# Performance work log

Measured on AMD Instinct MI355X. Metric: run time of the kernel, lower is better.

## Reference

```python
import jax, jax.numpy as jnp
import numpy as np

B, S, D = 16, 2048, 256
HEAD_SIZE = 256  # input_size // num_heads = 256 // 1
SCALE = HEAD_SIZE ** -0.5


def setup_inputs() -> dict:
    key = jax.random.key(0)
    ks = jax.random.split(key, 4)
    s = 1.0 / np.sqrt(D)  # typical linear init scale
    return {
        "x": jax.random.normal(ks[0], (B, S, D), dtype=jnp.float32),
        "Wq": jax.random.normal(ks[1], (D, D), dtype=jnp.float32) * s,
        "bq": jnp.zeros((D,), dtype=jnp.float32),
        "Wk": jax.random.normal(ks[2], (D, D), dtype=jnp.float32) * s,
        "bk": jnp.zeros((D,), dtype=jnp.float32),
        "Wv": jax.random.normal(ks[3], (D, D), dtype=jnp.float32) * s,
        "bv": jnp.zeros((D,), dtype=jnp.float32),
    }


def reference(x, Wq, bq, Wk, bk, Wv, bv):
    # Linear projections (torch Linear: x @ W.T + b)
    q = jnp.einsum("bsd,ed->bse", x, Wq) + bq
    k = jnp.einsum("bsd,ed->bse", x, Wk) + bk
    v = jnp.einsum("bsd,ed->bse", x, Wv) + bv
    # Full attention matrix [B, S, S], scaled by head_size^-0.5
    scores = jnp.einsum("bqd,bkd->bqk", q, k) * SCALE
    attn = jax.nn.softmax(scores, axis=-1)
    # dropout is identity in inference/reference mode
    out = jnp.einsum("bqk,bkd->bqd", attn, v)
    return out
```

## Files before the change

### kernel.cpp

```cpp
#include <hip/hip_runtime.h>
#include <hip/hip_bf16.h>
#include <stdint.h>

#define DEV __device__ __forceinline__

typedef __attribute__((ext_vector_type(8))) short bf16x8;
typedef __attribute__((ext_vector_type(4))) short bf16x4;
typedef __attribute__((ext_vector_type(4))) float f32x4;
typedef __attribute__((ext_vector_type(16))) float f32x16;
typedef unsigned short u16;

DEV void gload_lds16(const void* g, void* l) {
    typedef const __attribute__((address_space(1))) unsigned int* gp_t;
    typedef __attribute__((address_space(3))) unsigned int* lp_t;
    __builtin_amdgcn_global_load_lds((gp_t)(uintptr_t)g, (lp_t)(uint32_t)(uintptr_t)l, 16, 0, 0);
}

DEV u16 f2bf(float x) {
    union { __hip_bfloat16 h; u16 u; } c;
    c.h = __float2bfloat16(x);
    return c.u;
}
DEV unsigned pack2bf(float a, float b) {
    union { __hip_bfloat162 h2; unsigned u; } cv;
    cv.h2 = __float22bfloat162_rn(make_float2(a, b));
    return cv.u;
}
DEV float bflo(unsigned u) { union { unsigned u; float f; } c; c.u = u << 16; return c.f; }
DEV float bfhi(unsigned u) { union { unsigned u; float f; } c; c.u = u & 0xffff0000u; return c.f; }

DEV size_t kidx(int kv, int k) {
    return ((size_t)(kv >> 5) * 8192) + ((k >> 4) * 512)
         + (((((k >> 3) & 1) << 5) | (kv & 31)) << 3) + (k & 7);
}
DEV size_t vidx(int d, int kv) {
    return ((size_t)(kv >> 5) * 8192) + (((kv >> 3) & 3) * 2048) + ((d >> 5) * 256)
         + (((((kv >> 2) & 1) << 5) | (d & 31)) << 2) + (kv & 3);
}

__global__ void cast_kernel(const float* __restrict__ src, u16* __restrict__ dst, int n8) {
    int stride = gridDim.x * blockDim.x;
    for (int i = blockIdx.x * blockDim.x + threadIdx.x; i < n8; i += stride) {
        const float4* s = (const float4*)src + (size_t)i * 2;
        float4 a = s[0], b = s[1];
        union { u16 u[8]; uint4 v; } o;
        o.u[0] = f2bf(a.x); o.u[1] = f2bf(a.y); o.u[2] = f2bf(a.z); o.u[3] = f2bf(a.w);
        o.u[4] = f2bf(b.x); o.u[5] = f2bf(b.y); o.u[6] = f2bf(b.z); o.u[7] = f2bf(b.w);
        *((uint4*)dst + i) = o.v;
    }
}

template <int MODE>
DEV void gemm_body(const u16* A, const u16* Bw, const float* bias,
                   u16* out, int m0, int n0)
{
    __shared__ char smA[16384];
    __shared__ char smB[16384];
    const int lane = threadIdx.x & 63;
    const int w    = threadIdx.x >> 6;
    const int wr   = w >> 1, wc = w & 1;
    const int l15  = lane & 15, lg = lane >> 4;

    f32x4 acc[4][4] = {};
    const char* ag = (const char*)A;
    const char* bg = (const char*)Bw;

    for (int kt = 0; kt < 4; ++kt) {
        __syncthreads();
        #pragma unroll
        for (int c = 0; c < 8; ++c) {
            int ch    = w * 8 + c;
            int loc   = ch & 15;
            int p     = loc * 1024 + lane * 16;
            int row   = p >> 7;
            int inner = (p & 127) ^ ((row & 7) << 4);
            const char* src = (ch < 16 ? ag : bg) + row * 512 + kt * 128 + inner;
            char* dst = (ch < 16 ? smA : smB) + loc * 1024;
            gload_lds16(src, dst);
        }
        __syncthreads();
        #pragma unroll
        for (int ks = 0; ks < 2; ++ks) {
            bf16x8 af[4], bfr[4];
            #pragma unroll
            for (int mi = 0; mi < 4; ++mi) {
                int row = wr * 64 + mi * 16 + l15;
                af[mi] = *(const bf16x8*)(smA + ((row * 128 + ks * 64 + lg * 16) ^ ((row & 7) << 4)));
            }
            #pragma unroll
            for (int ni = 0; ni < 4; ++ni) {
                int row = wc * 64 + ni * 16 + l15;
                bfr[ni] = *(const bf16x8*)(smB + ((row * 128 + ks * 64 + lg * 16) ^ ((row & 7) << 4)));
            }
            #pragma unroll
            for (int mi = 0; mi < 4; ++mi)
                #pragma unroll
                for (int ni = 0; ni < 4; ++ni)
                    acc[mi][ni] = __builtin_amdgcn_mfma_f32_16x16x32_bf16(af[mi], bfr[ni], acc[mi][ni], 0, 0, 0);
        }
    }
    #pragma unroll
    for (int mi = 0; mi < 4; ++mi) {
        #pragma unroll
        for (int ni = 0; ni < 4; ++ni) {
            int gc = n0 + wc * 64 + ni * 16 + l15;
            float bc = (MODE == 2) ? 0.f : bias[gc];
            #pragma unroll
            for (int r = 0; r < 4; ++r) {
                int gr = m0 + wr * 64 + mi * 16 + lg * 4 + r;
                float bb = (MODE == 2) ? bias[gr] : bc;
                u16 val = f2bf(acc[mi][ni][r] + bb);
                if (MODE == 0)      out[(size_t)gr * 256 + gc] = val;
                else if (MODE == 1) out[kidx(gr, gc)] = val;
                else                out[vidx(gr, gc)] = val;
            }
        }
    }
}

__global__ __launch_bounds__(256) void proj_qk_kernel(
    const u16* xb, const u16* wqb, const u16* wkb,
    const float* bq, const float* bk, u16* Q, u16* Kf)
{
    int n0 = blockIdx.x * 128;
    int m0 = blockIdx.y * 128;
    int nl = n0 & 255;
    if (n0 < 256)
        gemm_body<0>(xb + (size_t)m0 * 256, wqb + (size_t)nl * 256, bq, Q,  m0, nl);
    else
        gemm_body<1>(xb + (size_t)m0 * 256, wkb + (size_t)nl * 256, bk, Kf, m0, nl);
}

__global__ __launch_bounds__(256) void proj_v_kernel(
    const u16* wvb, const u16* xb, const float* bv, u16* Vf)
{
    int n0 = blockIdx.x * 128;
    int m0 = blockIdx.y * 128;
    gemm_body<2>(wvb + (size_t)m0 * 256, xb + (size_t)n0 * 256, bv, Vf, m0, n0);
}

__global__ __launch_bounds__(256, 2) void attn_kernel(
    const u16* __restrict__ Q, const u16* __restrict__ Kf,
    const u16* __restrict__ Vf, float* __restrict__ out,
    u16* __restrict__ p1, float2* __restrict__ ml)
{
    __shared__ char sm[65536];

    const int lane = threadIdx.x & 63;
    const int w    = threadIdx.x >> 6;
    const int l31  = lane & 31;
    const int g    = lane >> 5;

    const int lin  = blockIdx.x;
    const int b    = (lin & 7) * 2 + ((lin >> 3) & 1);
    const int half = (lin >> 4) & 1;
    const int qt   = lin >> 5;
    const size_t tokbase = (size_t)b * 2048;
    const int q0w  = qt * 128 + w * 32;
    const int kvh  = half * 1024;

    bf16x8 qf[16];
    {
        const char* qrow = (const char*)(Q + (tokbase + q0w + l31) * 256);
        #pragma unroll
        for (int ks = 0; ks < 16; ++ks)
            qf[ks] = *(const bf16x8*)(qrow + ks * 32 + g * 16);
    }

    const char* Kgb = (const char*)Kf + (tokbase + kvh) * 512;
    const char* Vgb = (const char*)Vf + (tokbase + kvh) * 512;
    const uint32_t so = (uint32_t)(w * 4096 + lane * 16);

    auto stage = [&](int t, int sel) {
        const char* kg = Kgb + (size_t)t * 16384 + so;
        const char* vg = Vgb + (size_t)t * 16384 + so;
        char* kl = sm + sel * 32768 + w * 4096;
        char* vl = kl + 16384;
        #pragma unroll
        for (int j = 0; j < 4; ++j) gload_lds16(kg + j * 1024, kl + j * 1024);
        #pragma unroll
        for (int j = 0; j < 4; ++j) gload_lds16(vg + j * 1024, vl + j * 1024);
    };

    f32x16 acc[8] = {};
    float m_run  = -1e30f;
    float l_lane = 0.f;
    const float C = 0.09016844005556021f;

    stage(0, 0);
    __syncthreads();

    for (int t = 0; t < 32; ++t) {
        const int sel = t & 1;
        if (t < 31) stage(t + 1, sel ^ 1);

        const char* kp = sm + sel * 32768 + lane * 16;
        const char* vp = sm + sel * 32768 + 16384 + lane * 8;

        f32x16 sa = {}, sb = {};
        #pragma unroll
        for (int ks = 0; ks < 8; ++ks) {
            bf16x8 kf = *(const bf16x8*)(kp + ks * 1024);
            sa = __builtin_amdgcn_mfma_f32_32x32x16_bf16(kf, qf[ks], sa, 0, 0, 0);
        }
        #pragma unroll
        for (int ks = 8; ks < 16; ++ks) {
            bf16x8 kf = *(const bf16x8*)(kp + ks * 1024);
            sb = __builtin_amdgcn_mfma_f32_32x32x16_bf16(kf, qf[ks], sb, 0, 0, 0);
        }
        f32x16 st = sa + sb;

        float m0 = fmaxf(fmaxf(st[0], st[1]),   fmaxf(st[2], st[3]));
        float m1 = fmaxf(fmaxf(st[4], st[5]),   fmaxf(st[6], st[7]));
        float m2 = fmaxf(fmaxf(st[8], st[9]),   fmaxf(st[10], st[11]));
        float m3 = fmaxf(fmaxf(st[12], st[13]), fmaxf(st[14], st[15]));
        float lmax = fmaxf(fmaxf(m0, m1), fmaxf(m2, m3));

        if (__any(lmax > m_run + 16.f)) {
            float rmax = fmaxf(lmax, __shfl_xor(lmax, 32, 64));
            float m_new = fmaxf(m_run, rmax);
            float rs = exp2f((m_run - m_new) * C);
            #pragma unroll
            for (int dt = 0; dt < 8; ++dt) acc[dt] *= rs;
            l_lane *= rs;
            m_run = m_new;
        }

        const float mc = m_run * C;
        float sum = 0.f;
        #pragma unroll
        for (int i = 0; i < 16; ++i) {
            float e = exp2f(st[i] * C - mc);
            st[i] = e;
            sum += e;
        }
        l_lane += sum;

        union { unsigned u2[2]; bf16x4 v; } pb[4];
        #pragma unroll
        for (int u = 0; u < 4; ++u) {
            pb[u].u2[0] = pack2bf(st[u * 4 + 0], st[u * 4 + 1]);
            pb[u].u2[1] = pack2bf(st[u * 4 + 2], st[u * 4 + 3]);
        }

        #pragma unroll
        for (int u = 0; u < 4; ++u) {
            #pragma unroll
            for (int dt = 0; dt < 8; ++dt) {
                bf16x4 vf = *(const bf16x4*)(vp + u * 4096 + dt * 512);
                asm("v_mfma_f32_32x32x8_bf16 %0, %1, %2, %0"
                    : "+v"(acc[dt]) : "v"(vf), "v"(pb[u].v));
            }
        }

        __syncthreads();
    }

    float l_row = l_lane + __shfl_xor(l_lane, 32, 64);
    if (g == 0)
        ml[half * 32768 + (int)tokbase + q0w + l31] = make_float2(m_run, l_row);

    float* ow = (float*)(sm + w * 8448);
    #pragma unroll
    for (int p = 0; p < 4; ++p) {
        #pragma unroll
        for (int dt2 = 0; dt2 < 2; ++dt2) {
            const int dt = p * 2 + dt2;
            #pragma unroll
            for (int r = 0; r < 16; ++r) {
                int dl = dt2 * 32 + (r & 3) + 8 * (r >> 2) + 4 * g;
                ow[l31 * 66 + dl] = acc[dt][r];
            }
        }
        #pragma unroll
        for (int it = 0; it < 8; ++it) {
            int row = it * 4 + (lane >> 4);
            int dc  = (lane & 15) * 4;
            float2 lo = *(const float2*)(ow + row * 66 + dc);
            float2 hi = *(const float2*)(ow + row * 66 + dc + 2);
            if (half == 0) {
                float4 v; v.x = lo.x; v.y = lo.y; v.z = hi.x; v.w = hi.y;
                *(float4*)(out + (tokbase + q0w + row) * 256 + p * 64 + dc) = v;
            } else {
                uint2 pk2 = make_uint2(pack2bf(lo.x, lo.y), pack2bf(hi.x, hi.y));
                *(uint2*)(p1 + (tokbase + q0w + row) * 256 + p * 64 + dc) = pk2;
            }
        }
    }
}

__global__ __launch_bounds__(256) void combine_kernel(
    float* __restrict__ out, const u16* __restrict__ p1,
    const float2* __restrict__ ml)
{
    const float C = 0.09016844005556021f;
    int idx = blockIdx.x * 256 + threadIdx.x;
    int q = idx >> 5;
    int c = idx & 31;
    float2 h0 = ml[q];
    float2 h1 = ml[32768 + q];
    float M  = fmaxf(h0.x, h1.x);
    float k0 = exp2f((h0.x - M) * C);
    float k1 = exp2f((h1.x - M) * C);
    float inv = 1.f / (h0.y * k0 + h1.y * k1);
    k0 *= inv; k1 *= inv;
    size_t off = (size_t)q * 256 + c * 8;
    float4 a0 = *(const float4*)(out + off);
    float4 a1 = *(const float4*)(out + off + 4);
    uint2 u0 = *(const uint2*)(p1 + off);
    uint2 u1 = *(const uint2*)(p1 + off + 4);
    float4 r0, r1;
    r0.x = a0.x * k0 + bflo(u0.x) * k1;
    r0.y = a0.y * k0 + bfhi(u0.x) * k1;
    r0.z = a0.z * k0 + bflo(u0.y) * k1;
    r0.w = a0.w * k0 + bfhi(u0.y) * k1;
    r1.x = a1.x * k0 + bflo(u1.x) * k1;
    r1.y = a1.y * k0 + bfhi(u1.x) * k1;
    r1.z = a1.z * k0 + bflo(u1.y) * k1;
    r1.w = a1.w * k0 + bfhi(u1.y) * k1;
    *(float4*)(out + off)     = r0;
    *(float4*)(out + off + 4) = r1;
}

extern "C" void kernel_launch(void* const* d_in, const int* in_sizes, int n_in,
                              void* d_out, int out_size, void* d_ws, size_t ws_size,
                              hipStream_t stream) {
    (void)in_sizes; (void)n_in; (void)out_size; (void)ws_size;
    const float* x  = (const float*)d_in[0];
    const float* Wq = (const float*)d_in[1];
    const float* bq = (const float*)d_in[2];
    const float* Wk = (const float*)d_in[3];
    const float* bk = (const float*)d_in[4];
    const float* Wv = (const float*)d_in[5];
    const float* bv = (const float*)d_in[6];
    float* out = (float*)d_out;

    char* ws = (char*)d_ws;
    u16* xb  = (u16*)(ws);
    u16* wqb = (u16*)(ws + 16777216);
    u16* wkb = (u16*)(ws + 16908288);
    u16* wvb = (u16*)(ws + 17039360);
    u16* Qb  = (u16*)(ws + 17170432);
    u16* Kfr = (u16*)(ws + 33947648);
    u16* Vfr = (u16*)(ws + 50724864);
    float2* ml = (float2*)(ws + 67502080);

    cast_kernel<<<2048, 256, 0, stream>>>(x,  xb,  1048576);
    cast_kernel<<<64,   256, 0, stream>>>(Wq, wqb, 8192);
    cast_kernel<<<64,   256, 0, stream>>>(Wk, wkb, 8192);
    cast_kernel<<<64,   256, 0, stream>>>(Wv, wvb, 8192);

    proj_qk_kernel<<<dim3(4, 256), 256, 0, stream>>>(xb, wqb, wkb, bq, bk, Qb, Kfr);
    proj_v_kernel<<<dim3(256, 2), 256, 0, stream>>>(wvb, xb, bv, Vfr);

    attn_kernel<<<512, 256, 0, stream>>>(Qb, Kfr, Vfr, out, xb, ml);
    combine_kernel<<<4096, 256, 0, stream>>>(out, xb, ml);
}
```

Before: 166.2 us.

## Use 32x32x16 MFMA for PV, merge cast and projection launches

The P·V product now uses the K=16 bf16 MFMA with 8-element V fragments. The V layout is rearranged to match, and cross-half lane shuffles assemble the P operand, so each iteration issues half as many MFMAs and fewer, wider LDS reads. Separately, the four cast launches are merged into one kernel, and the Q/K and V projection kernels are merged into a single launch, to cut launch overhead and tail gaps. This adds four lane shuffles per iteration and a new V indexing scheme that must match the shuffled P layout exactly.

```diff
diff --git a/kernel.cpp b/kernel.cpp
--- a/kernel.cpp
+++ b/kernel.cpp
@@ -5,7 +5,6 @@
 #define DEV __device__ __forceinline__
 
 typedef __attribute__((ext_vector_type(8))) short bf16x8;
-typedef __attribute__((ext_vector_type(4))) short bf16x4;
 typedef __attribute__((ext_vector_type(4))) float f32x4;
 typedef __attribute__((ext_vector_type(16))) float f32x16;
 typedef unsigned short u16;
@@ -34,19 +33,34 @@
          + (((((k >> 3) & 1) << 5) | (kv & 31)) << 3) + (k & 7);
 }
 DEV size_t vidx(int d, int kv) {
-    return ((size_t)(kv >> 5) * 8192) + (((kv >> 3) & 3) * 2048) + ((d >> 5) * 256)
-         + (((((kv >> 2) & 1) << 5) | (d & 31)) << 2) + (kv & 3);
-}
-
-__global__ void cast_kernel(const float* __restrict__ src, u16* __restrict__ dst, int n8) {
+    return ((size_t)(kv >> 5) * 8192) + (((kv >> 4) & 1) * 4096) + ((d >> 5) * 512)
+         + (((((kv >> 3) & 1) << 5) | (d & 31)) << 3) + (kv & 7);
+}
+
+__global__ void cast_all_kernel(
+    const float* __restrict__ x,  const float* __restrict__ wq,
+    const float* __restrict__ wk, const float* __restrict__ wv,
+    u16* __restrict__ xb, u16* __restrict__ wqb,
+    u16* __restrict__ wkb, u16* __restrict__ wvb)
+{
+    const int total = 1048576 + 3 * 8192;
     int stride = gridDim.x * blockDim.x;
-    for (int i = blockIdx.x * blockDim.x + threadIdx.x; i < n8; i += stride) {
-        const float4* s = (const float4*)src + (size_t)i * 2;
-        float4 a = s[0], b = s[1];
+    for (int i = blockIdx.x * blockDim.x + threadIdx.x; i < total; i += stride) {
+        const float* s; u16* d; int off;
+        if (i < 1048576) { s = x; d = xb; off = i; }
+        else {
+            int j = i - 1048576;
+            int wsel = j >> 13;
+            off = j & 8191;
+            s = (wsel == 0) ? wq : (wsel == 1) ? wk : wv;
+            d = (wsel == 0) ? wqb : (wsel == 1) ? wkb : wvb;
+        }
+        const float4* sp = (const float4*)s + (size_t)off * 2;
+        float4 a = sp[0], b = sp[1];
         union { u16 u[8]; uint4 v; } o;
         o.u[0] = f2bf(a.x); o.u[1] = f2bf(a.y); o.u[2] = f2bf(a.z); o.u[3] = f2bf(a.w);
         o.u[4] = f2bf(b.x); o.u[5] = f2bf(b.y); o.u[6] = f2bf(b.z); o.u[7] = f2bf(b.w);
-        *((uint4*)dst + i) = o.v;
+        *((uint4*)d + off) = o.v;
     }
 }
 
@@ -118,25 +132,23 @@
     }
 }
 
-__global__ __launch_bounds__(256) void proj_qk_kernel(
-    const u16* xb, const u16* wqb, const u16* wkb,
-    const float* bq, const float* bk, u16* Q, u16* Kf)
-{
-    int n0 = blockIdx.x * 128;
+__global__ __launch_bounds__(256) void proj_all_kernel(
+    const u16* xb, const u16* wqb, const u16* wkb, const u16* wvb,
+    const float* bq, const float* bk, const float* bv,
+    u16* Q, u16* Kf, u16* Vf)
+{
+    int xg = blockIdx.x;
     int m0 = blockIdx.y * 128;
-    int nl = n0 & 255;
-    if (n0 < 256)
+    if (xg < 2) {
+        int nl = xg * 128;
         gemm_body<0>(xb + (size_t)m0 * 256, wqb + (size_t)nl * 256, bq, Q,  m0, nl);
-    else
+    } else if (xg < 4) {
+        int nl = (xg - 2) * 128;
         gemm_body<1>(xb + (size_t)m0 * 256, wkb + (size_t)nl * 256, bk, Kf, m0, nl);
-}
-
-__global__ __launch_bounds__(256) void proj_v_kernel(
-    const u16* wvb, const u16* xb, const float* bv, u16* Vf)
-{
-    int n0 = blockIdx.x * 128;
-    int m0 = blockIdx.y * 128;
-    gemm_body<2>(wvb + (size_t)m0 * 256, xb + (size_t)n0 * 256, bv, Vf, m0, n0);
+    } else {
+        int dm0 = (xg - 4) * 128;
+        gemm_body<2>(wvb + (size_t)dm0 * 256, xb + (size_t)m0 * 256, bv, Vf, dm0, m0);
+    }
 }
 
 __global__ __launch_bounds__(256, 2) void attn_kernel(
@@ -195,7 +207,7 @@
         if (t < 31) stage(t + 1, sel ^ 1);
 
         const char* kp = sm + sel * 32768 + lane * 16;
-        const char* vp = sm + sel * 32768 + 16384 + lane * 8;
+        const char* vp = sm + sel * 32768 + 16384 + lane * 16;
 
         f32x16 sa = {}, sb = {};
         #pragma unroll
@@ -236,21 +248,32 @@
         }
         l_lane += sum;
 
-        union { unsigned u2[2]; bf16x4 v; } pb[4];
-        #pragma unroll
-        for (int u = 0; u < 4; ++u) {
-            pb[u].u2[0] = pack2bf(st[u * 4 + 0], st[u * 4 + 1]);
-            pb[u].u2[1] = pack2bf(st[u * 4 + 2], st[u * 4 + 3]);
-        }
-
-        #pragma unroll
-        for (int u = 0; u < 4; ++u) {
-            #pragma unroll
-            for (int dt = 0; dt < 8; ++dt) {
-                bf16x4 vf = *(const bf16x4*)(vp + u * 4096 + dt * 512);
-                asm("v_mfma_f32_32x32x8_bf16 %0, %1, %2, %0"
-                    : "+v"(acc[dt]) : "v"(vf), "v"(pb[u].v));
-            }
+        unsigned pk0 = pack2bf(st[0], st[1]),   pk1 = pack2bf(st[2], st[3]);
+        unsigned pk2 = pack2bf(st[4], st[5]),   pk3 = pack2bf(st[6], st[7]);
+        unsigned pk4 = pack2bf(st[8], st[9]),   pk5 = pack2bf(st[10], st[11]);
+        unsigned pk6 = pack2bf(st[12], st[13]), pk7 = pack2bf(st[14], st[15]);
+
+        unsigned s0a = g ? pk0 : pk2,  s0b = g ? pk1 : pk3;
+        unsigned s1a = g ? pk4 : pk6,  s1b = g ? pk5 : pk7;
+        unsigned r0a = __shfl_xor(s0a, 32, 64);
+        unsigned r0b = __shfl_xor(s0b, 32, 64);
+        unsigned r1a = __shfl_xor(s1a, 32, 64);
+        unsigned r1b = __shfl_xor(s1b, 32, 64);
+        union { unsigned u[4]; bf16x8 v; } pB0, pB1;
+        pB0.u[0] = g ? r0a : pk0;  pB0.u[1] = g ? r0b : pk1;
+        pB0.u[2] = g ? pk2 : r0a;  pB0.u[3] = g ? pk3 : r0b;
+        pB1.u[0] = g ? r1a : pk4;  pB1.u[1] = g ? r1b : pk5;
+        pB1.u[2] = g ? pk6 : r1a;  pB1.u[3] = g ? pk7 : r1b;
+
+        #pragma unroll
+        for (int dt = 0; dt < 8; ++dt) {
+            bf16x8 v0 = *(const bf16x8*)(vp + dt * 1024);
+            acc[dt] = __builtin_amdgcn_mfma_f32_32x32x16_bf16(v0, pB0.v, acc[dt], 0, 0, 0);
+        }
+        #pragma unroll
+        for (int dt = 0; dt < 8; ++dt) {
+            bf16x8 v1 = *(const bf16x8*)(vp + 8192 + dt * 1024);
+            acc[dt] = __builtin_amdgcn_mfma_f32_32x32x16_bf16(v1, pB1.v, acc[dt], 0, 0, 0);
         }
 
         __syncthreads();
@@ -282,8 +305,8 @@
                 float4 v; v.x = lo.x; v.y = lo.y; v.z = hi.x; v.w = hi.y;
                 *(float4*)(out + (tokbase + q0w + row) * 256 + p * 64 + dc) = v;
             } else {
-                uint2 pk2 = make_uint2(pack2bf(lo.x, lo.y), pack2bf(hi.x, hi.y));
-                *(uint2*)(p1 + (tokbase + q0w + row) * 256 + p * 64 + dc) = pk2;
+                uint2 pk2v = make_uint2(pack2bf(lo.x, lo.y), pack2bf(hi.x, hi.y));
+                *(uint2*)(p1 + (tokbase + q0w + row) * 256 + p * 64 + dc) = pk2v;
             }
         }
     }
@@ -345,13 +368,10 @@
     u16* Vfr = (u16*)(ws + 50724864);
     float2* ml = (float2*)(ws + 67502080);
 
-    cast_kernel<<<2048, 256, 0, stream>>>(x,  xb,  1048576);
-    cast_kernel<<<64,   256, 0, stream>>>(Wq, wqb, 8192);
-    cast_kernel<<<64,   256, 0, stream>>>(Wk, wkb, 8192);
-    cast_kernel<<<64,   256, 0, stream>>>(Wv, wvb, 8192);
-
-    proj_qk_kernel<<<dim3(4, 256), 256, 0, stream>>>(xb, wqb, wkb, bq, bk, Qb, Kfr);
-    proj_v_kernel<<<dim3(256, 2), 256, 0, stream>>>(wvb, xb, bv, Vfr);
+    cast_all_kernel<<<2048, 256, 0, stream>>>(x, Wq, Wk, Wv, xb, wqb, wkb, wvb);
+
+    proj_all_kernel<<<dim3(6, 256), 256, 0, stream>>>(
+        xb, wqb, wkb, wvb, bq, bk, bv, Qb, Kfr, Vfr);
 
     attn_kernel<<<512, 256, 0, stream>>>(Qb, Kfr, Vfr, out, xb, ml);
     combine_kernel<<<4096, 256, 0, stream>>>(out, xb, ml);
```

Result: faster. 148.2 us (-10.8%).
